# Kernel optimization log

Hardware: AMD Instinct MI355X
Metric: run time of the kernel (lower is better)

## Reference

```python
import jax, jax.numpy as jnp
import numpy as np

B, T = 65536, 200
H, S, P = 512, 1000, 5
EPS = 1e-6


def setup_inputs() -> dict:
    key = jax.random.key(0)
    ks = jax.random.split(key, 8)
    init = lambda k, shp, fan: (jax.random.normal(k, shp, jnp.float32) / np.float32(np.sqrt(fan)))
    return {
        "X": jax.random.randint(ks[0], (B,), 0, S, dtype=jnp.int32),
        "y": jax.random.randint(ks[1], (B, T), 0, 2, dtype=jnp.int32),
        "embed": init(ks[2], (S, H), 1.0),
        "W1": init(ks[3], (H, H), H), "b1": jnp.zeros((H,), jnp.float32),
        "W2": init(ks[4], (H, H), H), "b2": jnp.zeros((H,), jnp.float32),
        "Wout": init(ks[5], (H, P), H), "bout": jnp.zeros((P,), jnp.float32),
    }


def reference(X, y, embed, W1, b1, W2, b2, Wout, bout):
    # --- MLP over skill embeddings: params (B, 5) = (l, f, g, s, latent0) ---
    e = embed[X]                                    # (B, H)
    h = jax.nn.relu(e @ W1 + b1)                    # num_layers = 2
    h = jax.nn.relu(h @ W2 + b2)
    params = jnp.clip(jax.nn.sigmoid(h @ Wout + bout), EPS, 1.0 - EPS)  # (B, 5)
    l, g, s = params[:, 0], params[:, 2], params[:, 3]
    latent0 = params[:, 4]                          # (B,)

    y_clean = jnp.where(y == -1, 0, y).astype(jnp.float32)  # (B, T)

    # --- BKT latent-update recurrence over T steps ---
    def step(latent, y_t):
        num1 = latent * (1.0 - s)
        correct = num1 + (1.0 - latent) * g
        k_t1 = num1 / correct
        k_t0 = latent * s / (latent * s + (1.0 - latent) * (1.0 - g))
        k_t = jnp.where(y_t > 0.5, k_t1, k_t0)
        nxt = jnp.clip(k_t + (1.0 - k_t) * l, EPS, 1.0 - EPS)
        return nxt, (correct, latent)

    _, (corrects, latents) = jax.lax.scan(step, latent0, y_clean.T)  # (T, B) each
    return corrects.T, latents.T, params
```

## Files before the change

### kernel.cpp

```cpp
#include <hip/hip_runtime.h>


typedef unsigned int uint;
typedef unsigned char uchar;
typedef unsigned short ushort_t;
typedef __attribute__((ext_vector_type(8))) short short8;
typedef __attribute__((ext_vector_type(4))) float f32x4;
typedef __attribute__((ext_vector_type(4))) uint uint4v;

#define SS 1000
#define HH 512
#define TT 200
#define BB_ 65536
#define PP 5

#define OFF_EMB   0
#define OFF_B1    512000
#define OFF_B2    512512
#define OFF_WOUT  513024
#define OFF_BOUT  515584
#define CONV_TOT  515589

__device__ __forceinline__ float b2f(ushort_t u) {
    return __uint_as_float(((uint)u) << 16);
}
__device__ __forceinline__ ushort_t f2b(float f) {
    uint u = __float_as_uint(f);
    uint r = u + 0x7FFFu + ((u >> 16) & 1u);
    return (ushort_t)(r >> 16);
}
__device__ __forceinline__ int detect_bf16(const uint* __restrict__ embed_raw,
                                           int tid) {
    uint w = embed_raw[tid & 63];
    uint e = (w >> 7) & 0xFFu;
    bool pl = (e >= 117u && e <= 130u);
    return __popcll(__ballot(pl)) >= 32 ? 1 : 0;
}
__device__ __forceinline__ ushort_t ld_bf16(const void* src, int idx, int fb) {
    return fb ? ((const ushort_t*)src)[idx] : f2b(((const float*)src)[idx]);
}

__device__ __forceinline__ float bkt_step(float latent, bool yt,
                                          float oms, float omg, float A1,
                                          float A0, float g, float s,
                                          float oml, float l,
                                          float* correct_out) {
    float num1    = latent * oms;
    float correct = fmaf(latent, A1, g);
    float lats    = latent * s;
    float num = yt ? num1 : lats;
    float den = yt ? correct : fmaf(latent, A0, omg);
    float kt  = num * __builtin_amdgcn_rcpf(den);
    *correct_out = correct;
    float nxt = fmaf(kt, oml, l);
    return fminf(fmaxf(nxt, 1e-6f), 1.f - 1e-6f);
}

__global__ __launch_bounds__(256) void prep_kernel(
    const void* __restrict__ embed, const void* __restrict__ W1,
    const void* __restrict__ b1,    const void* __restrict__ W2,
    const void* __restrict__ b2,    const void* __restrict__ Wout,
    const void* __restrict__ bout,
    ushort_t* __restrict__ conv, ushort_t* __restrict__ WT1,
    ushort_t* __restrict__ WT2)
{
    int tid = threadIdx.x;
    int fb = detect_bf16((const uint*)embed, tid);
    int bx = blockIdx.x;
    if (bx < 2015) {
        int i = bx * 256 + tid;
        if (i < CONV_TOT) {
            const void* src; int off;
            if      (i < OFF_B1)   { src = embed; off = i; }
            else if (i < OFF_B2)   { src = b1;    off = i - OFF_B1; }
            else if (i < OFF_WOUT) { src = b2;    off = i - OFF_B2; }
            else if (i < OFF_BOUT) { src = Wout;  off = i - OFF_WOUT; }
            else                   { src = bout;  off = i - OFF_BOUT; }
            conv[i] = ld_bf16(src, off, fb);
        }
    } else {
        __shared__ ushort_t t[32][33];
        int bi = bx - 2015;
        const void* W = bi < 256 ? W1 : W2;
        ushort_t* WT = bi < 256 ? WT1 : WT2;
        int ti = bi & 255;
        int k0 = (ti & 15) * 32, n0 = (ti >> 4) * 32;
        int tx = tid & 31, ty = tid >> 5;
        #pragma unroll
        for (int i = ty; i < 32; i += 8)
            t[i][tx] = ld_bf16(W, (k0 + i) * HH + n0 + tx, fb);
        __syncthreads();
        #pragma unroll
        for (int i = ty; i < 32; i += 8)
            WT[(n0 + i) * HH + k0 + tx] = t[tx][i];
    }
}

__global__ __launch_bounds__(256) void mlp_layer(
    const ushort_t* __restrict__ A, const ushort_t* __restrict__ WT,
    const ushort_t* __restrict__ bias, ushort_t* __restrict__ H, int Mclamp)
{
    int tid = threadIdx.x;
    int lane = tid & 63;
    int wave = tid >> 6;
    int m_base = blockIdx.x * 64 + wave * 16;
    int n_base = blockIdx.y * 16;
    int lrow = lane & 15;
    int q = lane >> 4;
    int rowA = m_base + lrow; if (rowA > Mclamp) rowA = Mclamp;

    const short8* Ap = (const short8*)(A + (size_t)rowA * HH) + q;
    const short8* Bp = (const short8*)(WT + (size_t)(n_base + lrow) * HH) + q;

    f32x4 acc = {0.f, 0.f, 0.f, 0.f};
    #pragma unroll 8
    for (int kk = 0; kk < 16; kk++) {
        short8 a = Ap[kk * 4];
        short8 b = Bp[kk * 4];
        acc = __builtin_amdgcn_mfma_f32_16x16x32_bf16(a, b, acc, 0, 0, 0);
    }

    int orow = m_base + q * 4;
    int n = n_base + lrow;
    float bb = b2f(bias[n]);
    #pragma unroll
    for (int r = 0; r < 4; r++) {
        float v = acc[r] + bb;
        H[(size_t)(orow + r) * HH + n] = f2b(fmaxf(v, 0.f));
    }
}

__global__ __launch_bounds__(256) void params_kernel(
    const ushort_t* __restrict__ h2, const ushort_t* __restrict__ conv,
    float* __restrict__ table)
{
    int wid = blockIdx.x * 4 + (threadIdx.x >> 6);
    int lane = threadIdx.x & 63;
    if (wid >= SS * PP) return;
    int row = wid / PP, p = wid - row * PP;
    const ushort_t* Wout = conv + OFF_WOUT;
    const ushort_t* bout = conv + OFF_BOUT;
    const short8* hr = (const short8*)(h2 + (size_t)row * HH);
    short8 h = hr[lane];
    float acc = 0.f;
    #pragma unroll
    for (int j = 0; j < 8; j++) {
        int k = lane * 8 + j;
        acc += b2f((ushort_t)h[j]) * b2f(Wout[k * PP + p]);
    }
    #pragma unroll
    for (int m = 32; m; m >>= 1) acc += __shfl_xor(acc, m);
    if (lane == 0) {
        float x = acc + b2f(bout[p]);
        float sg = 1.f / (1.f + expf(-x));
        sg = fminf(fmaxf(sg, 1e-6f), 1.f - 1e-6f);
        table[(size_t)row * 8 + p] = sg;
    }
}

__global__ __launch_bounds__(256) void scan_kernel(
    const int* __restrict__ X, const int* __restrict__ y,
    const float* __restrict__ table, const uint* __restrict__ embed_raw,
    void* __restrict__ out)
{
    __shared__ __align__(16) float stg[32 * 200];
    __shared__ uchar ybit[32 * 50];
    __shared__ float cpL[8 * 32];
    __shared__ uint  maskL[8 * 32];
    int tid = threadIdx.x;
    int rbase = blockIdx.x * 32;
    int fb = detect_bf16(embed_raw, tid);

    for (int idx = tid; idx < 1600; idx += 256) {
        int r = idx / 50, k = idx - r * 50;
        int4 v = *(const int4*)(y + (size_t)(rbase + r) * TT + k * 4);
        uint nib = (uint)(v.x == 1) | ((uint)(v.y == 1) << 1) |
                   ((uint)(v.z == 1) << 2) | ((uint)(v.w == 1) << 3);
        ybit[r * 50 + k] = (uchar)nib;
    }
    __syncthreads();

    if (tid < 32) {
        int rg = rbase + tid;
        int xi = X[rg]; xi = xi < 0 ? 0 : (xi >= SS ? SS - 1 : xi);
        float l      = table[xi * 8 + 0];
        float g      = table[xi * 8 + 2];
        float s      = table[xi * 8 + 3];
        float latent = table[xi * 8 + 4];
        float oms = 1.f - s, omg = 1.f - g, oml = 1.f - l;
        float A1 = 1.f - s - g, A0 = s + g - 1.f;
        int base = tid * 50;
        #pragma unroll
        for (int w = 0; w < 8; w++) {
            cpL[w * 32 + tid] = latent;
            uint m = 0;
            #pragma unroll
            for (int i = 0; i < 25; i++) {
                int t_ = w * 25 + i;
                uint bit = (ybit[base + (t_ >> 2)] >> (t_ & 3)) & 1u;
                m |= bit << i;
                float cd;
                latent = bkt_step(latent, bit, oms, omg, A1, A0, g, s, oml, l, &cd);
            }
            maskL[w * 32 + tid] = m;
        }
    }
    __syncthreads();

    int r = tid >> 3, j = tid & 7;
    int rg = rbase + r;
    int xi = X[rg]; xi = xi < 0 ? 0 : (xi >= SS ? SS - 1 : xi);
    float l  = table[xi * 8 + 0];
    float p1 = table[xi * 8 + 1];
    float g  = table[xi * 8 + 2];
    float s  = table[xi * 8 + 3];
    float L0 = table[xi * 8 + 4];

    if (j < 5) {
        float pv = j == 0 ? l : j == 1 ? p1 : j == 2 ? g : j == 3 ? s : L0;
        size_t po = 2ull * BB_ * TT + (size_t)rg * 5 + j;
        if (fb) ((ushort_t*)out)[po] = f2b(pv);
        else    ((float*)out)[po] = pv;
    }

    float latent = cpL[j * 32 + r];
    uint  u      = maskL[j * 32 + r];
    float oms = 1.f - s, omg = 1.f - g, oml = 1.f - l;
    float A1 = 1.f - s - g, A0 = s + g - 1.f;

    if (fb) {
        ushort_t* cgb = (ushort_t*)out;
        ushort_t* lgb = (ushort_t*)out + (size_t)BB_ * TT;
        size_t eoff = (size_t)rg * TT + j * 25;
        #pragma unroll
        for (int i = 0; i < 25; i++) {
            float correct;
            float nxt = bkt_step(latent, (u >> i) & 1u,
                                 oms, omg, A1, A0, g, s, oml, l, &correct);
            cgb[eoff + i] = f2b(correct);
            lgb[eoff + i] = f2b(latent);
            latent = nxt;
        }
        return;
    }

    float lat_arr[25];
    int sbase = r * 200 + j * 25;
    #pragma unroll
    for (int i = 0; i < 25; i++) {
        float correct;
        float nxt = bkt_step(latent, (u >> i) & 1u,
                             oms, omg, A1, A0, g, s, oml, l, &correct);
        stg[sbase + i] = correct;
        lat_arr[i] = latent;
        latent = nxt;
    }
    __syncthreads();
    {
        const uint4v* src = (const uint4v*)stg;
        uint4v* dst = (uint4v*)((float*)out + (size_t)rbase * TT);
        for (int idx = tid; idx < 1600; idx += 256)
            __builtin_nontemporal_store(src[idx], dst + idx);
    }
    __syncthreads();
    #pragma unroll
    for (int i = 0; i < 25; i++)
        stg[sbase + i] = lat_arr[i];
    __syncthreads();
    {
        const uint4v* src = (const uint4v*)stg;
        uint4v* dst = (uint4v*)((float*)out + (size_t)BB_ * TT + (size_t)rbase * TT);
        for (int idx = tid; idx < 1600; idx += 256)
            __builtin_nontemporal_store(src[idx], dst + idx);
    }
}

extern "C" void kernel_launch(void* const* d_in, const int* in_sizes, int n_in,
                              void* d_out, int out_size, void* d_ws, size_t ws_size,
                              hipStream_t stream) {
    const int* X = (const int*)d_in[0];
    const int* y = (const int*)d_in[1];

    char* ws = (char*)d_ws;
    ushort_t* conv  = (ushort_t*)(ws);
    ushort_t* WT1   = (ushort_t*)(ws + 1048576);
    ushort_t* WT2   = (ushort_t*)(ws + 1572864);
    ushort_t* h1    = (ushort_t*)(ws + 2097152);
    ushort_t* h2    = (ushort_t*)(ws + 3145728);
    float*    table = (float*)(ws + 4194304);

    prep_kernel<<<dim3(2527, 1, 1), 256, 0, stream>>>(
        d_in[2], d_in[3], d_in[4], d_in[5], d_in[6], d_in[7], d_in[8],
        conv, WT1, WT2);
    mlp_layer<<<dim3(16, 32, 1), 256, 0, stream>>>(conv + OFF_EMB, WT1, conv + OFF_B1, h1, SS - 1);
    mlp_layer<<<dim3(16, 32, 1), 256, 0, stream>>>(h1, WT2, conv + OFF_B2, h2, 1023);
    params_kernel<<<dim3(1250, 1, 1), 256, 0, stream>>>(h2, conv, table);
    scan_kernel<<<dim3(2048, 1, 1), 256, 0, stream>>>(
        X, y, table, (const uint*)d_in[2], (void*)d_out);
}
```

Measured before the change: 204.0 us.

## Compute scan once, derive correct from stored latents, and vectorize prep conversion

After: 212.2 us. 4.0% more time.

```diff
diff --git a/kernel.cpp b/kernel.cpp
--- a/kernel.cpp
+++ b/kernel.cpp
@@ -6,7 +6,7 @@
 typedef unsigned short ushort_t;
 typedef __attribute__((ext_vector_type(8))) short short8;
 typedef __attribute__((ext_vector_type(4))) float f32x4;
-typedef __attribute__((ext_vector_type(4))) uint uint4v;
+typedef __attribute__((ext_vector_type(2))) uint uint2v;
 
 #define SS 1000
 #define HH 512
@@ -43,15 +43,13 @@
 __device__ __forceinline__ float bkt_step(float latent, bool yt,
                                           float oms, float omg, float A1,
                                           float A0, float g, float s,
-                                          float oml, float l,
-                                          float* correct_out) {
+                                          float oml, float l) {
     float num1    = latent * oms;
     float correct = fmaf(latent, A1, g);
     float lats    = latent * s;
     float num = yt ? num1 : lats;
     float den = yt ? correct : fmaf(latent, A0, omg);
     float kt  = num * __builtin_amdgcn_rcpf(den);
-    *correct_out = correct;
     float nxt = fmaf(kt, oml, l);
     return fminf(fmaxf(nxt, 1e-6f), 1.f - 1e-6f);
 }
@@ -67,8 +65,8 @@
     int tid = threadIdx.x;
     int fb = detect_bf16((const uint*)embed, tid);
     int bx = blockIdx.x;
-    if (bx < 2015) {
-        int i = bx * 256 + tid;
+    if (bx < 504) {
+        int i = (bx * 256 + tid) * 4;
         if (i < CONV_TOT) {
             const void* src; int off;
             if      (i < OFF_B1)   { src = embed; off = i; }
@@ -76,11 +74,25 @@
             else if (i < OFF_WOUT) { src = b2;    off = i - OFF_B2; }
             else if (i < OFF_BOUT) { src = Wout;  off = i - OFF_WOUT; }
             else                   { src = bout;  off = i - OFF_BOUT; }
-            conv[i] = ld_bf16(src, off, fb);
+            if (i + 3 < CONV_TOT) {
+                ushort_t o0, o1, o2, o3;
+                if (fb) {
+                    ushort4 v = *(const ushort4*)((const ushort_t*)src + off);
+                    o0 = v.x; o1 = v.y; o2 = v.z; o3 = v.w;
+                } else {
+                    float4 v = *(const float4*)((const float*)src + off);
+                    o0 = f2b(v.x); o1 = f2b(v.y); o2 = f2b(v.z); o3 = f2b(v.w);
+                }
+                ushort4 o; o.x = o0; o.y = o1; o.z = o2; o.w = o3;
+                *(ushort4*)(conv + i) = o;
+            } else {
+                for (int k = 0; i + k < CONV_TOT; k++)
+                    conv[i + k] = ld_bf16(src, off + k, fb);
+            }
         }
     } else {
         __shared__ ushort_t t[32][33];
-        int bi = bx - 2015;
+        int bi = bx - 504;
         const void* W = bi < 256 ? W1 : W2;
         ushort_t* WT = bi < 256 ? WT1 : WT2;
         int ti = bi & 255;
@@ -165,8 +177,7 @@
 {
     __shared__ __align__(16) float stg[32 * 200];
     __shared__ uchar ybit[32 * 50];
-    __shared__ float cpL[8 * 32];
-    __shared__ uint  maskL[8 * 32];
+    __shared__ float pA1[32], pG[32];
     int tid = threadIdx.x;
     int rbase = blockIdx.x * 32;
     int fb = detect_bf16(embed_raw, tid);
@@ -174,104 +185,78 @@
     for (int idx = tid; idx < 1600; idx += 256) {
         int r = idx / 50, k = idx - r * 50;
         int4 v = *(const int4*)(y + (size_t)(rbase + r) * TT + k * 4);
-        uint nib = (uint)(v.x == 1) | ((uint)(v.y == 1) << 1) |
-                   ((uint)(v.z == 1) << 2) | ((uint)(v.w == 1) << 3);
-        ybit[r * 50 + k] = (uchar)nib;
+        ybit[r * 50 + k] = (uchar)((uint)(v.x == 1) | ((uint)(v.y == 1) << 1) |
+                                   ((uint)(v.z == 1) << 2) | ((uint)(v.w == 1) << 3));
     }
     __syncthreads();
 
-    if (tid < 32) {
-        int rg = rbase + tid;
+    int lane = tid & 63, wv = tid >> 6;
+    if (lane < 8) {
+        int r = wv * 8 + lane;
+        int rg = rbase + r;
         int xi = X[rg]; xi = xi < 0 ? 0 : (xi >= SS ? SS - 1 : xi);
         float l      = table[xi * 8 + 0];
+        float p1     = table[xi * 8 + 1];
         float g      = table[xi * 8 + 2];
         float s      = table[xi * 8 + 3];
-        float latent = table[xi * 8 + 4];
+        float L0     = table[xi * 8 + 4];
         float oms = 1.f - s, omg = 1.f - g, oml = 1.f - l;
         float A1 = 1.f - s - g, A0 = s + g - 1.f;
-        int base = tid * 50;
-        #pragma unroll
-        for (int w = 0; w < 8; w++) {
-            cpL[w * 32 + tid] = latent;
-            uint m = 0;
+        pA1[r] = A1; pG[r] = g;
+
+        if (fb) {
+            ushort_t* pp = (ushort_t*)out + 2ull * BB_ * TT + (size_t)rg * 5;
+            pp[0] = f2b(l); pp[1] = f2b(p1); pp[2] = f2b(g);
+            pp[3] = f2b(s); pp[4] = f2b(L0);
+        } else {
+            float* pp = (float*)out + 2ull * BB_ * TT + (size_t)rg * 5;
+            pp[0] = l; pp[1] = p1; pp[2] = g; pp[3] = s; pp[4] = L0;
+        }
+
+        float latent = L0;
+        const uchar* yb = &ybit[r * 50];
+        float* srow = &stg[r * 200];
+        for (int k = 0; k < 50; k++) {
+            uint nib = yb[k];
             #pragma unroll
-            for (int i = 0; i < 25; i++) {
-                int t_ = w * 25 + i;
-                uint bit = (ybit[base + (t_ >> 2)] >> (t_ & 3)) & 1u;
-                m |= bit << i;
-                float cd;
-                latent = bkt_step(latent, bit, oms, omg, A1, A0, g, s, oml, l, &cd);
+            for (int i = 0; i < 4; i++) {
+                srow[k * 4 + i] = latent;
+                latent = bkt_step(latent, (nib >> i) & 1u,
+                                  oms, omg, A1, A0, g, s, oml, l);
             }
-            maskL[w * 32 + tid] = m;
         }
     }
     __syncthreads();
 
-    int r = tid >> 3, j = tid & 7;
-    int rg = rbase + r;
-    int xi = X[rg]; xi = xi < 0 ? 0 : (xi >= SS ? SS - 1 : xi);
-    float l  = table[xi * 8 + 0];
-    float p1 = table[xi * 8 + 1];
-    float g  = table[xi * 8 + 2];
-    float s  = table[xi * 8 + 3];
-    float L0 = table[xi * 8 + 4];
-
-    if (j < 5) {
-        float pv = j == 0 ? l : j == 1 ? p1 : j == 2 ? g : j == 3 ? s : L0;
-        size_t po = 2ull * BB_ * TT + (size_t)rg * 5 + j;
-        if (fb) ((ushort_t*)out)[po] = f2b(pv);
-        else    ((float*)out)[po] = pv;
-    }
-
-    float latent = cpL[j * 32 + r];
-    uint  u      = maskL[j * 32 + r];
-    float oms = 1.f - s, omg = 1.f - g, oml = 1.f - l;
-    float A1 = 1.f - s - g, A0 = s + g - 1.f;
-
-    if (fb) {
-        ushort_t* cgb = (ushort_t*)out;
-        ushort_t* lgb = (ushort_t*)out + (size_t)BB_ * TT;
-        size_t eoff = (size_t)rg * TT + j * 25;
-        #pragma unroll
-        for (int i = 0; i < 25; i++) {
-            float correct;
-            float nxt = bkt_step(latent, (u >> i) & 1u,
-                                 oms, omg, A1, A0, g, s, oml, l, &correct);
-            cgb[eoff + i] = f2b(correct);
-            lgb[eoff + i] = f2b(latent);
-            latent = nxt;
-        }
-        return;
-    }
-
-    float lat_arr[25];
-    int sbase = r * 200 + j * 25;
-    #pragma unroll
-    for (int i = 0; i < 25; i++) {
-        float correct;
-        float nxt = bkt_step(latent, (u >> i) & 1u,
-                             oms, omg, A1, A0, g, s, oml, l, &correct);
-        stg[sbase + i] = correct;
-        lat_arr[i] = latent;
-        latent = nxt;
-    }
-    __syncthreads();
-    {
-        const uint4v* src = (const uint4v*)stg;
-        uint4v* dst = (uint4v*)((float*)out + (size_t)rbase * TT);
-        for (int idx = tid; idx < 1600; idx += 256)
-            __builtin_nontemporal_store(src[idx], dst + idx);
-    }
-    __syncthreads();
-    #pragma unroll
-    for (int i = 0; i < 25; i++)
-        stg[sbase + i] = lat_arr[i];
-    __syncthreads();
-    {
-        const uint4v* src = (const uint4v*)stg;
-        uint4v* dst = (uint4v*)((float*)out + (size_t)BB_ * TT + (size_t)rbase * TT);
-        for (int idx = tid; idx < 1600; idx += 256)
-            __builtin_nontemporal_store(src[idx], dst + idx);
+    const f32x4* src = (const f32x4*)stg;
+    if (!fb) {
+        f32x4* dc = (f32x4*)((float*)out + (size_t)rbase * TT);
+        f32x4* dl = (f32x4*)((float*)out + (size_t)BB_ * TT + (size_t)rbase * TT);
+        for (int idx = tid; idx < 1600; idx += 256) {
+            int r = idx / 50;
+            f32x4 v = src[idx];
+            float A1 = pA1[r], g = pG[r];
+            f32x4 c;
+            c[0] = fmaf(v[0], A1, g); c[1] = fmaf(v[1], A1, g);
+            c[2] = fmaf(v[2], A1, g); c[3] = fmaf(v[3], A1, g);
+            __builtin_nontemporal_store(v, dl + idx);
+            __builtin_nontemporal_store(c, dc + idx);
+        }
+    } else {
+        uint2v* dc = (uint2v*)((ushort_t*)out + (size_t)rbase * TT);
+        uint2v* dl = (uint2v*)((ushort_t*)out + (size_t)BB_ * TT + (size_t)rbase * TT);
+        for (int idx = tid; idx < 1600; idx += 256) {
+            int r = idx / 50;
+            f32x4 v = src[idx];
+            float A1 = pA1[r], g = pG[r];
+            uint2v lv, cv;
+            lv[0] = (uint)f2b(v[0]) | ((uint)f2b(v[1]) << 16);
+            lv[1] = (uint)f2b(v[2]) | ((uint)f2b(v[3]) << 16);
+            cv[0] = (uint)f2b(fmaf(v[0], A1, g)) | ((uint)f2b(fmaf(v[1], A1, g)) << 16);
+            cv[1] = (uint)f2b(fmaf(v[2], A1, g)) | ((uint)f2b(fmaf(v[3], A1, g)) << 16);
+            __builtin_nontemporal_store(lv, dl + idx);
+            __builtin_nontemporal_store(cv, dc + idx);
+        }
     }
 }
 
@@ -289,7 +274,7 @@
     ushort_t* h2    = (ushort_t*)(ws + 3145728);
     float*    table = (float*)(ws + 4194304);
 
-    prep_kernel<<<dim3(2527, 1, 1), 256, 0, stream>>>(
+    prep_kernel<<<dim3(1016, 1, 1), 256, 0, stream>>>(
         d_in[2], d_in[3], d_in[4], d_in[5], d_in[6], d_in[7], d_in[8],
         conv, WT1, WT2);
     mlp_layer<<<dim3(16, 32, 1), 256, 0, stream>>>(conv + OFF_EMB, WT1, conv + OFF_B1, h1, SS - 1);
```
